# Performance work log

Hardware: AMD Instinct MI355X
Metric: run time of the kernel (lower is better)

Reference implementation:

```python
import jax, jax.numpy as jnp
import numpy as np

B, S, DIM, H = 8, 1024, 1024, 16
D = DIM // H  # d_head = 64


def setup_inputs() -> dict:
    key = jax.random.key(0)
    ks = jax.random.split(key, 7)
    scale = 1.0 / np.sqrt(D)  # nn.Linear default init range ~ U(-1/sqrt(in), 1/sqrt(in))
    x = jax.random.normal(ks[0], (B, S, DIM), dtype=jnp.float32)
    Wq = jax.random.uniform(ks[1], (H, D, D), jnp.float32, -scale, scale)
    Wk = jax.random.uniform(ks[2], (H, D, D), jnp.float32, -scale, scale)
    Wv = jax.random.uniform(ks[3], (H, D, D), jnp.float32, -scale, scale)
    bq = jax.random.uniform(ks[4], (H, D), jnp.float32, -scale, scale)
    bk = jax.random.uniform(ks[5], (H, D), jnp.float32, -scale, scale)
    bv = jax.random.uniform(ks[6], (H, D), jnp.float32, -scale, scale)
    return {"x": x, "Wq": Wq, "Wk": Wk, "Wv": Wv, "bq": bq, "bk": bk, "bv": bv}


def reference(x, Wq, Wk, Wv, bq, bk, bv):
    # x: [B,S,DIM] -> split heads: [B,S,H,D] (matches per-head column slicing)
    xh = x.reshape(x.shape[0], x.shape[1], H, D)
    # per-head linear: y = x @ W.T + b  (nn.Linear convention: weight [out,in])
    q = jnp.einsum('bshd,hed->bshe', xh, Wq) + bq  # [B,S,H,D]
    k = jnp.einsum('bshd,hed->bshe', xh, Wk) + bk
    v = jnp.einsum('bshd,hed->bshe', xh, Wv) + bv
    scores = jnp.einsum('bqhd,bkhd->bhqk', q, k) / jnp.sqrt(jnp.float32(D))
    attn = jax.nn.softmax(scores, axis=-1)  # [B,H,S,S]
    out = jnp.einsum('bhqk,bkhd->bqhd', attn, v)  # [B,S,H,D]
    # hstack over heads == merge last two dims back to DIM
    return out.reshape(x.shape[0], x.shape[1], H * D)
```

## Files before the change

### kernel.cpp

```cpp
#include <hip/hip_runtime.h>
#include <hip/hip_bf16.h>

#define BB 8
#define SS 1024
#define HH 16
#define DD 64
#define DIMM 1024
#define NUNITS (BB * HH)
#define UNIT_ELEMS (SS * DD)
#define NW (3 * HH * DD * DD)

typedef __attribute__((ext_vector_type(8))) short short8;
typedef __attribute__((ext_vector_type(4))) float f32x4;

__device__ inline short f2b(float f) {
    unsigned u = __float_as_uint(f);
    u = (u + 0x7FFFu + ((u >> 16) & 1u)) >> 16;
    return (short)u;
}
__device__ inline unsigned pk2(float lo, float hi) {
    unsigned a = __float_as_uint(lo), b = __float_as_uint(hi);
    a = (a + 0x7FFFu + ((a >> 16) & 1u)) >> 16;
    b = (b + 0x7FFFu + ((b >> 16) & 1u)) & 0xFFFF0000u;
    return a | b;
}

__global__ __launch_bounds__(256) void wconv(
    const float* __restrict__ Wq, const float* __restrict__ Wk,
    const float* __restrict__ Wv, short* __restrict__ Wb)
{
    int idx = (blockIdx.x * 256 + threadIdx.x) * 8;
    if (idx >= NW) return;
    int m = idx >> 16;
    int r = idx & 65535;
    const float* src = (m == 0) ? Wq : (m == 1) ? Wk : Wv;
    float4 a = *reinterpret_cast<const float4*>(src + r);
    float4 b = *reinterpret_cast<const float4*>(src + r + 4);
    short8 o;
    o[0] = f2b(a.x); o[1] = f2b(a.y); o[2] = f2b(a.z); o[3] = f2b(a.w);
    o[4] = f2b(b.x); o[5] = f2b(b.y); o[6] = f2b(b.z); o[7] = f2b(b.w);
    *reinterpret_cast<short8*>(Wb + idx) = o;
}

__global__ __launch_bounds__(256) void qkv_proj(
    const float* __restrict__ x, const short* __restrict__ Wb,
    const float* __restrict__ bqp, const float* __restrict__ bkp,
    const float* __restrict__ bvp,
    short* __restrict__ Qo, short* __restrict__ Ko, short* __restrict__ Vto,
    int unit0)
{
    __shared__ alignas(16) short wsm[3][64][72];
    __shared__ alignas(16) short xs[64][72];

    const int t = threadIdx.x;
    const int bid = blockIdx.x;
    const int st = bid & 15;
    const int ul = bid >> 4;
    const int unit = unit0 + ul;
    const int h = unit & 15;
    const int b = unit >> 4;
    const int s0 = st * 64;

    for (int m = 0; m < 3; ++m)
        for (int i = 0; i < 2; ++i) {
            int g = t + i * 256;
            int row = g >> 3, col = (g & 7) * 8;
            *reinterpret_cast<short8*>(&wsm[m][row][col]) =
                *reinterpret_cast<const short8*>(Wb + ((size_t)(m * HH + h)) * 4096 + row * 64 + col);
        }
    for (int i = 0; i < 4; ++i) {
        int g = t + i * 256;
        int r = g >> 4, c = (g & 15) * 4;
        float4 xv = *reinterpret_cast<const float4*>(
            x + ((size_t)(b * SS + s0 + r)) * DIMM + h * DD + c);
        short4 sv; sv.x = f2b(xv.x); sv.y = f2b(xv.y); sv.z = f2b(xv.z); sv.w = f2b(xv.w);
        *reinterpret_cast<short4*>(&xs[r][c]) = sv;
    }
    __syncthreads();

    const int lane = t & 63, w = t >> 6;
    const int l15 = lane & 15, quad = lane >> 4;

    short8 a0 = *reinterpret_cast<const short8*>(&xs[w * 16 + l15][quad * 8]);
    short8 a1 = *reinterpret_cast<const short8*>(&xs[w * 16 + l15][32 + quad * 8]);

    #pragma unroll 1
    for (int m = 0; m < 3; ++m) {
        f32x4 a_[4];
        for (int et = 0; et < 4; ++et) {
            short8 w0 = *reinterpret_cast<const short8*>(&wsm[m][et * 16 + l15][quad * 8]);
            short8 w1 = *reinterpret_cast<const short8*>(&wsm[m][et * 16 + l15][32 + quad * 8]);
            f32x4 a = {0.f, 0.f, 0.f, 0.f};
            a = __builtin_amdgcn_mfma_f32_16x16x32_bf16(a0, w0, a, 0, 0, 0);
            a = __builtin_amdgcn_mfma_f32_16x16x32_bf16(a1, w1, a, 0, 0, 0);
            a_[et] = a;
        }
        __syncthreads();
        const float* bp = (m == 0) ? bqp : (m == 1) ? bkp : bvp;
        const float scale = (m == 0) ? 0.125f : 1.0f;
        for (int et = 0; et < 4; ++et) {
            float bias = bp[h * DD + et * 16 + l15];
            int e = et * 16 + l15;
            for (int r = 0; r < 4; ++r) {
                float v = (a_[et][r] + bias) * scale;
                int srow = w * 16 + quad * 4 + r;
                if (m == 2) wsm[2][e][srow] = f2b(v);
                else        wsm[m][srow][e] = f2b(v);
            }
        }
    }
    __syncthreads();

    for (int m = 0; m < 3; ++m)
        for (int i = 0; i < 2; ++i) {
            int g = t + i * 256;
            int row = g >> 3, col = (g & 7) * 8;
            short8 val = *reinterpret_cast<const short8*>(&wsm[m][row][col]);
            if (m == 0)
                *reinterpret_cast<short8*>(Qo + ((size_t)ul * SS + s0 + row) * DD + col) = val;
            else if (m == 1)
                *reinterpret_cast<short8*>(Ko + ((size_t)ul * SS + s0 + row) * DD + col) = val;
            else
                *reinterpret_cast<short8*>(Vto + ((size_t)ul * DD + row) * SS + s0 + col) = val;
        }
}

__global__ __launch_bounds__(256, 4) void attn(
    const short* __restrict__ Q, const short* __restrict__ K,
    const short* __restrict__ Vt, float* __restrict__ out, int unit0, int nu)
{
    __shared__ alignas(16) short ks[64][72];
    __shared__ alignas(16) short vts[64][72];
    __shared__ alignas(16) short ps[4][32][72];

    const int t = threadIdx.x;
    const int bid = blockIdx.x;
    int ul, qt;
    if (nu == NUNITS) {
        int xslot = bid & 7;
        int j = bid >> 3;
        ul = xslot * 16 + (j & 15);
        qt = j >> 4;
    } else {
        ul = bid >> 3;
        qt = bid & 7;
    }
    const int unit = unit0 + ul;
    const int h = unit & 15;
    const int b = unit >> 4;
    const int q0 = qt * 128;
    const int lane = t & 63, w = t >> 6;
    const int l15 = lane & 15, quad = lane >> 4;

    short8 qa[2][2];
    for (int s = 0; s < 2; ++s) {
        const short* qp = Q + ((size_t)ul * SS + q0 + s * 64 + w * 16 + l15) * DD;
        qa[s][0] = *reinterpret_cast<const short8*>(qp + quad * 8);
        qa[s][1] = *reinterpret_cast<const short8*>(qp + 32 + quad * 8);
    }

    short8 ones;
    for (int j = 0; j < 8; ++j) ones[j] = (short)0x3F80;

    f32x4 o[8];
    f32x4 lacc[2];
    for (int i = 0; i < 8; ++i) o[i] = (f32x4){0.f, 0.f, 0.f, 0.f};
    lacc[0] = (f32x4){0.f, 0.f, 0.f, 0.f};
    lacc[1] = (f32x4){0.f, 0.f, 0.f, 0.f};

    const int srow_ = t >> 3, scol = (t & 7) * 8;

    const float L2E = 1.44269504f;
    const float MBIAS = 11.5415603f;

    for (int kt = 0; kt < 16; ++kt) {
        const int k0 = kt * 64;
        __syncthreads();
        for (int i = 0; i < 2; ++i) {
            int row = srow_ + i * 32;
            *reinterpret_cast<short8*>(&ks[row][scol]) =
                *reinterpret_cast<const short8*>(K + ((size_t)ul * SS + k0 + row) * DD + scol);
            *reinterpret_cast<short8*>(&vts[row][scol]) =
                *reinterpret_cast<const short8*>(Vt + ((size_t)ul * DD + row) * SS + k0 + scol);
        }
        __syncthreads();

        for (int n = 0; n < 4; ++n) {
            short8 kb0 = *reinterpret_cast<const short8*>(&ks[n * 16 + l15][quad * 8]);
            short8 kb1 = *reinterpret_cast<const short8*>(&ks[n * 16 + l15][32 + quad * 8]);
            for (int s = 0; s < 2; ++s) {
                f32x4 a = {0.f, 0.f, 0.f, 0.f};
                a = __builtin_amdgcn_mfma_f32_16x16x32_bf16(kb0, qa[s][0], a, 0, 0, 0);
                a = __builtin_amdgcn_mfma_f32_16x16x32_bf16(kb1, qa[s][1], a, 0, 0, 0);
                float p0 = exp2f(fmaf(a[0], L2E, -MBIAS));
                float p1 = exp2f(fmaf(a[1], L2E, -MBIAS));
                float p2 = exp2f(fmaf(a[2], L2E, -MBIAS));
                float p3 = exp2f(fmaf(a[3], L2E, -MBIAS));
                uint2 pk; pk.x = pk2(p0, p1); pk.y = pk2(p2, p3);
                *reinterpret_cast<uint2*>(&ps[w][s * 16 + l15][n * 16 + quad * 4]) = pk;
            }
        }

        short8 pa[2][2];
        for (int s = 0; s < 2; ++s) {
            pa[s][0] = *reinterpret_cast<const short8*>(&ps[w][s * 16 + l15][quad * 8]);
            pa[s][1] = *reinterpret_cast<const short8*>(&ps[w][s * 16 + l15][32 + quad * 8]);
            lacc[s] = __builtin_amdgcn_mfma_f32_16x16x32_bf16(pa[s][0], ones, lacc[s], 0, 0, 0);
            lacc[s] = __builtin_amdgcn_mfma_f32_16x16x32_bf16(pa[s][1], ones, lacc[s], 0, 0, 0);
        }
        for (int dt = 0; dt < 4; ++dt) {
            short8 vb0 = *reinterpret_cast<const short8*>(&vts[dt * 16 + l15][quad * 8]);
            short8 vb1 = *reinterpret_cast<const short8*>(&vts[dt * 16 + l15][32 + quad * 8]);
            for (int s = 0; s < 2; ++s) {
                o[s * 4 + dt] = __builtin_amdgcn_mfma_f32_16x16x32_bf16(pa[s][0], vb0, o[s * 4 + dt], 0, 0, 0);
                o[s * 4 + dt] = __builtin_amdgcn_mfma_f32_16x16x32_bf16(pa[s][1], vb1, o[s * 4 + dt], 0, 0, 0);
            }
        }
    }

    for (int s = 0; s < 2; ++s)
        for (int dt = 0; dt < 4; ++dt)
            for (int r = 0; r < 4; ++r) {
                int srow = q0 + s * 64 + w * 16 + quad * 4 + r;
                int col = h * DD + dt * 16 + l15;
                out[((size_t)b * SS + srow) * DIMM + col] = o[s * 4 + dt][r] / lacc[s][r];
            }
}

extern "C" void kernel_launch(void* const* d_in, const int* in_sizes, int n_in,
                              void* d_out, int out_size, void* d_ws, size_t ws_size,
                              hipStream_t stream) {
    const float* x   = (const float*)d_in[0];
    const float* Wq  = (const float*)d_in[1];
    const float* Wk  = (const float*)d_in[2];
    const float* Wv  = (const float*)d_in[3];
    const float* bqp = (const float*)d_in[4];
    const float* bkp = (const float*)d_in[5];
    const float* bvp = (const float*)d_in[6];
    float* out = (float*)d_out;

    short* Wb = (short*)d_ws;
    const size_t w_elems = NW;
    const size_t unit_bytes = 3ULL * UNIT_ELEMS * sizeof(short);
    size_t avail = ws_size > w_elems * 2 ? ws_size - w_elems * 2 : 0;
    int U = (int)(avail / unit_bytes);
    if (U < 1) U = 1;
    if (U > NUNITS) U = NUNITS;

    short* Qw  = Wb + w_elems;
    short* Kw  = Qw + (size_t)U * UNIT_ELEMS;
    short* Vtw = Kw + (size_t)U * UNIT_ELEMS;

    wconv<<<dim3((NW / 8 + 255) / 256), dim3(256), 0, stream>>>(Wq, Wk, Wv, Wb);

    for (int u0 = 0; u0 < NUNITS; u0 += U) {
        int nu = NUNITS - u0 < U ? NUNITS - u0 : U;
        qkv_proj<<<dim3(nu * 16), dim3(256), 0, stream>>>(
            x, Wb, bqp, bkp, bvp, Qw, Kw, Vtw, u0);
        attn<<<dim3(nu * 8), dim3(256), 0, stream>>>(Qw, Kw, Vtw, out, u0, nu);
    }
}
```

Baseline: 165.4 us.

## Fuse weight conversion into projection, loop seq tiles per block, micro-opt attention

Drops the separate weight-conversion kernel. The projection kernel now loads fp32 weights and converts them to bf16 in shared memory, then reuses them across four 64-row sequence tiles per block, so the grid has a quarter as many blocks. The attention kernel uses precomputed pointer increments and hardware exp2/rcp builtins, and multiplies by a reciprocal in the epilogue instead of dividing. This cuts one launch, redundant weight loads and some address arithmetic, at the cost of fewer projection blocks and an extra shared buffer.

```diff
diff --git a/kernel.cpp b/kernel.cpp
--- a/kernel.cpp
+++ b/kernel.cpp
@@ -8,10 +8,20 @@
 #define DIMM 1024
 #define NUNITS (BB * HH)
 #define UNIT_ELEMS (SS * DD)
-#define NW (3 * HH * DD * DD)
 
 typedef __attribute__((ext_vector_type(8))) short short8;
 typedef __attribute__((ext_vector_type(4))) float f32x4;
+
+#if __has_builtin(__builtin_amdgcn_exp2f)
+#define EXP2F(x) __builtin_amdgcn_exp2f(x)
+#else
+#define EXP2F(x) exp2f(x)
+#endif
+#if __has_builtin(__builtin_amdgcn_rcpf)
+#define RCPF(x) __builtin_amdgcn_rcpf(x)
+#else
+#define RCPF(x) (1.0f / (x))
+#endif
 
 __device__ inline short f2b(float f) {
     unsigned u = __float_as_uint(f);
@@ -25,25 +35,9 @@
     return a | b;
 }
 
-__global__ __launch_bounds__(256) void wconv(
-    const float* __restrict__ Wq, const float* __restrict__ Wk,
-    const float* __restrict__ Wv, short* __restrict__ Wb)
-{
-    int idx = (blockIdx.x * 256 + threadIdx.x) * 8;
-    if (idx >= NW) return;
-    int m = idx >> 16;
-    int r = idx & 65535;
-    const float* src = (m == 0) ? Wq : (m == 1) ? Wk : Wv;
-    float4 a = *reinterpret_cast<const float4*>(src + r);
-    float4 b = *reinterpret_cast<const float4*>(src + r + 4);
-    short8 o;
-    o[0] = f2b(a.x); o[1] = f2b(a.y); o[2] = f2b(a.z); o[3] = f2b(a.w);
-    o[4] = f2b(b.x); o[5] = f2b(b.y); o[6] = f2b(b.z); o[7] = f2b(b.w);
-    *reinterpret_cast<short8*>(Wb + idx) = o;
-}
-
 __global__ __launch_bounds__(256) void qkv_proj(
-    const float* __restrict__ x, const short* __restrict__ Wb,
+    const float* __restrict__ x, const float* __restrict__ Wq,
+    const float* __restrict__ Wk, const float* __restrict__ Wv,
     const float* __restrict__ bqp, const float* __restrict__ bkp,
     const float* __restrict__ bvp,
     short* __restrict__ Qo, short* __restrict__ Ko, short* __restrict__ Vto,
@@ -51,78 +45,85 @@
 {
     __shared__ alignas(16) short wsm[3][64][72];
     __shared__ alignas(16) short xs[64][72];
+    __shared__ alignas(16) short tr[64][72];
 
     const int t = threadIdx.x;
     const int bid = blockIdx.x;
-    const int st = bid & 15;
-    const int ul = bid >> 4;
+    const int stg = bid & 3;
+    const int ul = bid >> 2;
     const int unit = unit0 + ul;
     const int h = unit & 15;
     const int b = unit >> 4;
-    const int s0 = st * 64;
-
-    for (int m = 0; m < 3; ++m)
-        for (int i = 0; i < 2; ++i) {
+
+    for (int m = 0; m < 3; ++m) {
+        const float* src = ((m == 0) ? Wq : (m == 1) ? Wk : Wv) + h * DD * DD;
+        for (int i = 0; i < 4; ++i) {
             int g = t + i * 256;
-            int row = g >> 3, col = (g & 7) * 8;
-            *reinterpret_cast<short8*>(&wsm[m][row][col]) =
-                *reinterpret_cast<const short8*>(Wb + ((size_t)(m * HH + h)) * 4096 + row * 64 + col);
-        }
-    for (int i = 0; i < 4; ++i) {
-        int g = t + i * 256;
-        int r = g >> 4, c = (g & 15) * 4;
-        float4 xv = *reinterpret_cast<const float4*>(
-            x + ((size_t)(b * SS + s0 + r)) * DIMM + h * DD + c);
-        short4 sv; sv.x = f2b(xv.x); sv.y = f2b(xv.y); sv.z = f2b(xv.z); sv.w = f2b(xv.w);
-        *reinterpret_cast<short4*>(&xs[r][c]) = sv;
-    }
-    __syncthreads();
+            int e = g >> 4, c = (g & 15) * 4;
+            float4 wv = *reinterpret_cast<const float4*>(src + e * DD + c);
+            short4 sv; sv.x = f2b(wv.x); sv.y = f2b(wv.y); sv.z = f2b(wv.z); sv.w = f2b(wv.w);
+            *reinterpret_cast<short4*>(&wsm[m][e][c]) = sv;
+        }
+    }
 
     const int lane = t & 63, w = t >> 6;
     const int l15 = lane & 15, quad = lane >> 4;
 
-    short8 a0 = *reinterpret_cast<const short8*>(&xs[w * 16 + l15][quad * 8]);
-    short8 a1 = *reinterpret_cast<const short8*>(&xs[w * 16 + l15][32 + quad * 8]);
-
-    #pragma unroll 1
-    for (int m = 0; m < 3; ++m) {
-        f32x4 a_[4];
-        for (int et = 0; et < 4; ++et) {
-            short8 w0 = *reinterpret_cast<const short8*>(&wsm[m][et * 16 + l15][quad * 8]);
-            short8 w1 = *reinterpret_cast<const short8*>(&wsm[m][et * 16 + l15][32 + quad * 8]);
-            f32x4 a = {0.f, 0.f, 0.f, 0.f};
-            a = __builtin_amdgcn_mfma_f32_16x16x32_bf16(a0, w0, a, 0, 0, 0);
-            a = __builtin_amdgcn_mfma_f32_16x16x32_bf16(a1, w1, a, 0, 0, 0);
-            a_[et] = a;
+    for (int st2 = 0; st2 < 4; ++st2) {
+        const int s0 = (stg * 4 + st2) * 64;
+        if (st2) __syncthreads();
+        for (int i = 0; i < 4; ++i) {
+            int g = t + i * 256;
+            int r = g >> 4, c = (g & 15) * 4;
+            float4 xv = *reinterpret_cast<const float4*>(
+                x + ((size_t)(b * SS + s0 + r)) * DIMM + h * DD + c);
+            short4 sv; sv.x = f2b(xv.x); sv.y = f2b(xv.y); sv.z = f2b(xv.z); sv.w = f2b(xv.w);
+            *reinterpret_cast<short4*>(&xs[r][c]) = sv;
         }
         __syncthreads();
-        const float* bp = (m == 0) ? bqp : (m == 1) ? bkp : bvp;
-        const float scale = (m == 0) ? 0.125f : 1.0f;
-        for (int et = 0; et < 4; ++et) {
-            float bias = bp[h * DD + et * 16 + l15];
-            int e = et * 16 + l15;
-            for (int r = 0; r < 4; ++r) {
-                float v = (a_[et][r] + bias) * scale;
-                int srow = w * 16 + quad * 4 + r;
-                if (m == 2) wsm[2][e][srow] = f2b(v);
-                else        wsm[m][srow][e] = f2b(v);
-            }
-        }
-    }
-    __syncthreads();
-
-    for (int m = 0; m < 3; ++m)
-        for (int i = 0; i < 2; ++i) {
-            int g = t + i * 256;
-            int row = g >> 3, col = (g & 7) * 8;
-            short8 val = *reinterpret_cast<const short8*>(&wsm[m][row][col]);
-            if (m == 0)
-                *reinterpret_cast<short8*>(Qo + ((size_t)ul * SS + s0 + row) * DD + col) = val;
-            else if (m == 1)
-                *reinterpret_cast<short8*>(Ko + ((size_t)ul * SS + s0 + row) * DD + col) = val;
-            else
-                *reinterpret_cast<short8*>(Vto + ((size_t)ul * DD + row) * SS + s0 + col) = val;
-        }
+
+        short8 a0 = *reinterpret_cast<const short8*>(&xs[w * 16 + l15][quad * 8]);
+        short8 a1 = *reinterpret_cast<const short8*>(&xs[w * 16 + l15][32 + quad * 8]);
+
+        f32x4 acc[12];
+        for (int m = 0; m < 3; ++m)
+            for (int et = 0; et < 4; ++et) {
+                short8 w0 = *reinterpret_cast<const short8*>(&wsm[m][et * 16 + l15][quad * 8]);
+                short8 w1 = *reinterpret_cast<const short8*>(&wsm[m][et * 16 + l15][32 + quad * 8]);
+                f32x4 a = {0.f, 0.f, 0.f, 0.f};
+                a = __builtin_amdgcn_mfma_f32_16x16x32_bf16(a0, w0, a, 0, 0, 0);
+                a = __builtin_amdgcn_mfma_f32_16x16x32_bf16(a1, w1, a, 0, 0, 0);
+                acc[m * 4 + et] = a;
+            }
+
+        for (int m = 0; m < 3; ++m) {
+            if (m) __syncthreads();
+            const float* bp = (m == 0) ? bqp : (m == 1) ? bkp : bvp;
+            const float scale = (m == 0) ? 0.125f : 1.0f;
+            for (int et = 0; et < 4; ++et) {
+                float bias = bp[h * DD + et * 16 + l15];
+                int e = et * 16 + l15;
+                for (int r = 0; r < 4; ++r) {
+                    float v = (acc[m * 4 + et][r] + bias) * scale;
+                    int srow = w * 16 + quad * 4 + r;
+                    if (m == 2) tr[e][srow] = f2b(v);
+                    else        tr[srow][e] = f2b(v);
+                }
+            }
+            __syncthreads();
+            for (int i = 0; i < 2; ++i) {
+                int g = t + i * 256;
+                int row = g >> 3, col = (g & 7) * 8;
+                short8 val = *reinterpret_cast<const short8*>(&tr[row][col]);
+                if (m == 0)
+                    *reinterpret_cast<short8*>(Qo + ((size_t)ul * SS + s0 + row) * DD + col) = val;
+                else if (m == 1)
+                    *reinterpret_cast<short8*>(Ko + ((size_t)ul * SS + s0 + row) * DD + col) = val;
+                else
+                    *reinterpret_cast<short8*>(Vto + ((size_t)ul * DD + row) * SS + s0 + col) = val;
+            }
+        }
+    }
 }
 
 __global__ __launch_bounds__(256, 4) void attn(
@@ -170,47 +171,54 @@
 
     const int srow_ = t >> 3, scol = (t & 7) * 8;
 
+    const short* kg = K + (size_t)ul * UNIT_ELEMS + srow_ * DD + scol;
+    const short* vg = Vt + (size_t)ul * UNIT_ELEMS + srow_ * SS + scol;
+    char* ksw = (char*)&ks[srow_][scol];
+    char* vtw = (char*)&vts[srow_][scol];
+    const char* kbp = (const char*)&ks[l15][quad * 8];
+    const char* vbp = (const char*)&vts[l15][quad * 8];
+    const char* pap = (const char*)&ps[w][l15][quad * 8];
+    char* psw = (char*)&ps[w][l15][quad * 4];
+
     const float L2E = 1.44269504f;
     const float MBIAS = 11.5415603f;
 
     for (int kt = 0; kt < 16; ++kt) {
-        const int k0 = kt * 64;
         __syncthreads();
-        for (int i = 0; i < 2; ++i) {
-            int row = srow_ + i * 32;
-            *reinterpret_cast<short8*>(&ks[row][scol]) =
-                *reinterpret_cast<const short8*>(K + ((size_t)ul * SS + k0 + row) * DD + scol);
-            *reinterpret_cast<short8*>(&vts[row][scol]) =
-                *reinterpret_cast<const short8*>(Vt + ((size_t)ul * DD + row) * SS + k0 + scol);
-        }
+        *reinterpret_cast<short8*>(ksw) = *reinterpret_cast<const short8*>(kg);
+        *reinterpret_cast<short8*>(ksw + 32 * 144) = *reinterpret_cast<const short8*>(kg + 32 * DD);
+        *reinterpret_cast<short8*>(vtw) = *reinterpret_cast<const short8*>(vg);
+        *reinterpret_cast<short8*>(vtw + 32 * 144) = *reinterpret_cast<const short8*>(vg + 32 * SS);
+        kg += 64 * DD;
+        vg += 64;
         __syncthreads();
 
         for (int n = 0; n < 4; ++n) {
-            short8 kb0 = *reinterpret_cast<const short8*>(&ks[n * 16 + l15][quad * 8]);
-            short8 kb1 = *reinterpret_cast<const short8*>(&ks[n * 16 + l15][32 + quad * 8]);
+            short8 kb0 = *reinterpret_cast<const short8*>(kbp + n * 2304);
+            short8 kb1 = *reinterpret_cast<const short8*>(kbp + n * 2304 + 64);
             for (int s = 0; s < 2; ++s) {
                 f32x4 a = {0.f, 0.f, 0.f, 0.f};
                 a = __builtin_amdgcn_mfma_f32_16x16x32_bf16(kb0, qa[s][0], a, 0, 0, 0);
                 a = __builtin_amdgcn_mfma_f32_16x16x32_bf16(kb1, qa[s][1], a, 0, 0, 0);
-                float p0 = exp2f(fmaf(a[0], L2E, -MBIAS));
-                float p1 = exp2f(fmaf(a[1], L2E, -MBIAS));
-                float p2 = exp2f(fmaf(a[2], L2E, -MBIAS));
-                float p3 = exp2f(fmaf(a[3], L2E, -MBIAS));
+                float p0 = EXP2F(fmaf(a[0], L2E, -MBIAS));
+                float p1 = EXP2F(fmaf(a[1], L2E, -MBIAS));
+                float p2 = EXP2F(fmaf(a[2], L2E, -MBIAS));
+                float p3 = EXP2F(fmaf(a[3], L2E, -MBIAS));
                 uint2 pk; pk.x = pk2(p0, p1); pk.y = pk2(p2, p3);
-                *reinterpret_cast<uint2*>(&ps[w][s * 16 + l15][n * 16 + quad * 4]) = pk;
+                *reinterpret_cast<uint2*>(psw + s * 2304 + n * 32) = pk;
             }
         }
 
         short8 pa[2][2];
         for (int s = 0; s < 2; ++s) {
-            pa[s][0] = *reinterpret_cast<const short8*>(&ps[w][s * 16 + l15][quad * 8]);
-            pa[s][1] = *reinterpret_cast<const short8*>(&ps[w][s * 16 + l15][32 + quad * 8]);
+            pa[s][0] = *reinterpret_cast<const short8*>(pap + s * 2304);
+            pa[s][1] = *reinterpret_cast<const short8*>(pap + s * 2304 + 64);
             lacc[s] = __builtin_amdgcn_mfma_f32_16x16x32_bf16(pa[s][0], ones, lacc[s], 0, 0, 0);
             lacc[s] = __builtin_amdgcn_mfma_f32_16x16x32_bf16(pa[s][1], ones, lacc[s], 0, 0, 0);
         }
         for (int dt = 0; dt < 4; ++dt) {
-            short8 vb0 = *reinterpret_cast<const short8*>(&vts[dt * 16 + l15][quad * 8]);
-            short8 vb1 = *reinterpret_cast<const short8*>(&vts[dt * 16 + l15][32 + quad * 8]);
+            short8 vb0 = *reinterpret_cast<const short8*>(vbp + dt * 2304);
+            short8 vb1 = *reinterpret_cast<const short8*>(vbp + dt * 2304 + 64);
             for (int s = 0; s < 2; ++s) {
                 o[s * 4 + dt] = __builtin_amdgcn_mfma_f32_16x16x32_bf16(pa[s][0], vb0, o[s * 4 + dt], 0, 0, 0);
                 o[s * 4 + dt] = __builtin_amdgcn_mfma_f32_16x16x32_bf16(pa[s][1], vb1, o[s * 4 + dt], 0, 0, 0);
@@ -218,13 +226,13 @@
         }
     }
 
+    float* outp = out + ((size_t)b * SS + q0 + w * 16 + quad * 4) * DIMM + h * DD + l15;
     for (int s = 0; s < 2; ++s)
-        for (int dt = 0; dt < 4; ++dt)
-            for (int r = 0; r < 4; ++r) {
-                int srow = q0 + s * 64 + w * 16 + quad * 4 + r;
-                int col = h * DD + dt * 16 + l15;
-                out[((size_t)b * SS + srow) * DIMM + col] = o[s * 4 + dt][r] / lacc[s][r];
-            }
+        for (int r = 0; r < 4; ++r) {
+            float rin = RCPF(lacc[s][r]);
+            for (int dt = 0; dt < 4; ++dt)
+                outp[(size_t)(s * 64 + r) * DIMM + dt * 16] = o[s * 4 + dt][r] * rin;
+        }
 }
 
 extern "C" void kernel_launch(void* const* d_in, const int* in_sizes, int n_in,
@@ -239,24 +247,19 @@
     const float* bvp = (const float*)d_in[6];
     float* out = (float*)d_out;
 
-    short* Wb = (short*)d_ws;
-    const size_t w_elems = NW;
     const size_t unit_bytes = 3ULL * UNIT_ELEMS * sizeof(short);
-    size_t avail = ws_size > w_elems * 2 ? ws_size - w_elems * 2 : 0;
-    int U = (int)(avail / unit_bytes);
+    int U = (int)(ws_size / unit_bytes);
     if (U < 1) U = 1;
     if (U > NUNITS) U = NUNITS;
 
-    short* Qw  = Wb + w_elems;
+    short* Qw  = (short*)d_ws;
     short* Kw  = Qw + (size_t)U * UNIT_ELEMS;
     short* Vtw = Kw + (size_t)U * UNIT_ELEMS;
 
-    wconv<<<dim3((NW / 8 + 255) / 256), dim3(256), 0, stream>>>(Wq, Wk, Wv, Wb);
-
     for (int u0 = 0; u0 < NUNITS; u0 += U) {
         int nu = NUNITS - u0 < U ? NUNITS - u0 : U;
-        qkv_proj<<<dim3(nu * 16), dim3(256), 0, stream>>>(
-            x, Wb, bqp, bkp, bvp, Qw, Kw, Vtw, u0);
+        qkv_proj<<<dim3(nu * 4), dim3(256), 0, stream>>>(
+            x, Wq, Wk, Wv, bqp, bkp, bvp, Qw, Kw, Vtw, u0);
         attn<<<dim3(nu * 8), dim3(256), 0, stream>>>(Qw, Kw, Vtw, out, u0, nu);
     }
 }
```

Result: faster. 152.6 us (-7.8%).
